# Kernel optimization log

Hardware: AMD Instinct MI355X
Metric: run time of the kernel (lower is better)

Reference implementation:

```python
import math
import jax, jax.numpy as jnp
import numpy as np

B, S, H, D = 2, 2048, 16, 64

def setup_inputs() -> dict:
    key = jax.random.key(0)
    qkv = jax.random.normal(key, (B, S, 3, H, D), dtype=jnp.float32)
    return {"qkv": qkv}

def reference(qkv) -> jnp.ndarray:
    # qkv: [B, S, 3, H, D]
    q = qkv[:, :, 0]  # [B, S, H, D]
    k = qkv[:, :, 1]
    v = qkv[:, :, 2]
    seqlen = qkv.shape[1]
    softmax_scale = 1.0 / math.sqrt(q.shape[-1])
    # scores: [B, H, T, S]
    scores = jnp.einsum('bthd,bshd->bhts', q, k * softmax_scale)
    # additive causal mask with -10000 above the diagonal (matches torch.triu(..., 1))
    causal_mask = jnp.triu(jnp.full((seqlen, seqlen), -10000.0, dtype=scores.dtype), 1)
    scores = scores + causal_mask
    attention = jax.nn.softmax(scores, axis=-1)
    # dropout_p = 0.0 (eval), so no dropout applied
    output = jnp.einsum('bhts,bshd->bthd', attention, v)  # [B, T, H, D]
    return output
```

## Files before the change

### kernel.cpp

```cpp
#include <hip/hip_runtime.h>

typedef __bf16 bf16x8 __attribute__((ext_vector_type(8)));
typedef float f32x4 __attribute__((ext_vector_type(4)));
typedef unsigned int u32;

constexpr int Bc = 2, Sc = 2048, Hc = 16, Dc = 64;
constexpr int QBLK = 64, KVBLK = 64;
constexpr int NT = Sc / QBLK;
constexpr int ROWSTR = 3 * Hc * Dc;
constexpr float QSCALE = 0.125f * 1.4426950408889634f;


template <int CTRL>
static __device__ __forceinline__ float dppf(float x) {
  int xi = __builtin_bit_cast(int, x);
  return __builtin_bit_cast(float,
      __builtin_amdgcn_update_dpp(xi, xi, CTRL, 0xF, 0xF, false));
}
static __device__ __forceinline__ float redmax16(float x) {
  x = fmaxf(x, dppf<0x121>(x));
  x = fmaxf(x, dppf<0x122>(x));
  x = fmaxf(x, dppf<0x124>(x));
  x = fmaxf(x, dppf<0x128>(x));
  return x;
}
static __device__ __forceinline__ float redsum16(float x) {
  x += dppf<0x121>(x);
  x += dppf<0x122>(x);
  x += dppf<0x124>(x);
  x += dppf<0x128>(x);
  return x;
}

static __device__ __forceinline__ u32 pack2(float a, float b) {
  unsigned short x = __builtin_bit_cast(unsigned short, (__bf16)a);
  unsigned short y = __builtin_bit_cast(unsigned short, (__bf16)b);
  return (u32)x | ((u32)y << 16);
}

__global__ __launch_bounds__(512, 4)
void fattn_kernel(const float* __restrict__ qkv, float* __restrict__ out) {
  const int id = blockIdx.x + blockIdx.y * gridDim.x;
  const int swz = (id & 7) * 64 + (id >> 3);
  const int xlow = swz & 15;
  const int xhigh = NT - 1 - xlow;
  const int bh = swz >> 4;
  const int b = bh >> 4, h = bh & 15;

  const int tid = threadIdx.x;
  const int wave = tid >> 6;
  const int lane = tid & 63;
  const int lg = lane >> 4;
  const int li = lane & 15;
  const bool is_h = wave < 4;
  const int sub = wave & 3;
  const int myx = is_h ? xhigh : xlow;
  const int qw = myx * QBLK + sub * 16;

  const float* qp = qkv + (size_t)b * Sc * ROWSTR + h * Dc;
  const float* kp = qp + Hc * Dc;
  const float* vp = qp + 2 * Hc * Dc;

  __shared__ __align__(16) char k_s[KVBLK * Dc * 2];
  __shared__ __align__(16) char v_s[Dc * KVBLK * 2];
  __shared__ __align__(16) char p_s[8][16 * KVBLK * 2];
  char* pw = p_s[wave];

  bf16x8 qf[2];
  {
    const float* qr = qp + (size_t)(qw + li) * ROWSTR + 8 * lg;
#pragma unroll
    for (int fi = 0; fi < 2; ++fi) {
      f32x4 a0 = *(const f32x4*)(qr + 32 * fi);
      f32x4 a1 = *(const f32x4*)(qr + 32 * fi + 4);
      bf16x8 qa;
#pragma unroll
      for (int j = 0; j < 4; ++j) {
        qa[j] = (__bf16)(a0[j] * QSCALE); qa[j + 4] = (__bf16)(a1[j] * QSCALE);
      }
      qf[fi] = qa;
    }
  }

  f32x4 oacc[4];
  float mrow[4], lrow[4];
#pragma unroll
  for (int n = 0; n < 4; ++n) oacc[n] = f32x4{0, 0, 0, 0};
#pragma unroll
  for (int r = 0; r < 4; ++r) { mrow[r] = -1e30f; lrow[r] = 0.f; }

  for (int t = 0; t <= xhigh; ++t) {
    const int kv0 = t * KVBLK;

    {
      const int r = tid >> 3, g = tid & 7;
      const float* ks = kp + (size_t)(kv0 + r) * ROWSTR + g * 8;
      const float* vs = vp + (size_t)(kv0 + r) * ROWSTR + g * 8;
      f32x4 k0 = *(const f32x4*)ks;
      f32x4 k1 = *(const f32x4*)(ks + 4);
      f32x4 v0 = *(const f32x4*)vs;
      f32x4 v1 = *(const f32x4*)(vs + 4);
      bf16x8 kb;
#pragma unroll
      for (int j = 0; j < 4; ++j) { kb[j] = (__bf16)k0[j]; kb[j + 4] = (__bf16)k1[j]; }
      *(bf16x8*)(k_s + ((r * 128 + g * 16) ^ ((r & 7) << 4))) = kb;

      const int odd = r & 1;
      f32x4 tmp = odd ? v0 : v1;
      f32x4 rcv;
#pragma unroll
      for (int j = 0; j < 4; ++j) rcv[j] = dppf<0x128>(tmp[j]);
      const int kvb2 = (r & ~1) * 2;
#pragma unroll
      for (int s = 0; s < 4; ++s) {
        const int dj = (s + g) & 3;
        const float lo = odd ? rcv[dj] : v0[dj];
        const float hi = odd ? v1[dj] : rcv[dj];
        const int d = 8 * g + 4 * odd + dj;
        *(u32*)(v_s + ((d * 128 + kvb2) ^ ((d & 7) << 4))) = pack2(lo, hi);
      }
    }
    __syncthreads();

    if (t <= myx) {
      f32x4 sacc[4];
#pragma unroll
      for (int n = 0; n < 4; ++n) sacc[n] = f32x4{0, 0, 0, 0};
      __builtin_amdgcn_s_setprio(1);
#pragma unroll
      for (int n = 0; n < 4; ++n) {
        const int krow = 16 * n + li;
        const int sw = (krow & 7) << 4;
#pragma unroll
        for (int fi = 0; fi < 2; ++fi) {
          bf16x8 kb = *(const bf16x8*)(k_s + ((krow * 128 + fi * 64 + lg * 16) ^ sw));
          sacc[n] = __builtin_amdgcn_mfma_f32_16x16x32_bf16(qf[fi], kb, sacc[n], 0, 0, 0);
        }
      }
      __builtin_amdgcn_s_setprio(0);

      if (t == myx) {
        const int qrow = qw + 4 * lg;
#pragma unroll
        for (int n = 0; n < 4; ++n)
#pragma unroll
          for (int r = 0; r < 4; ++r)
            if (kv0 + 16 * n + li > qrow + r) sacc[n][r] = -1e30f;
      }

      float pm[4];
#pragma unroll
      for (int r = 0; r < 4; ++r) {
        pm[r] = fmaxf(fmaxf(sacc[0][r], sacc[1][r]), fmaxf(sacc[2][r], sacc[3][r]));
        pm[r] = redmax16(pm[r]);
      }

      bool need = false;
#pragma unroll
      for (int r = 0; r < 4; ++r) need = need || (pm[r] > mrow[r] + 8.0f);
      if (__any(need)) {
#pragma unroll
        for (int r = 0; r < 4; ++r) {
          float mnew = fmaxf(mrow[r], pm[r]);
          float scl = __builtin_exp2f(mrow[r] - mnew);
          mrow[r] = mnew;
          lrow[r] *= scl;
#pragma unroll
          for (int n = 0; n < 4; ++n) oacc[n][r] *= scl;
        }
      }

#pragma unroll
      for (int r = 0; r < 4; ++r) {
        float s = 0.f;
#pragma unroll
        for (int n = 0; n < 4; ++n) {
          float p = __builtin_exp2f(sacc[n][r] - mrow[r]);
          sacc[n][r] = p;
          s += p;
        }
        lrow[r] += redsum16(s);
      }

      {
        const int oddli = li & 1;
        const int kvoff = (li & ~1) * 2;
        const int q0 = 4 * lg + 2 * oddli;
        const int sw0 = (q0 & 7) << 4;
        const int sw1 = ((q0 + 1) & 7) << 4;
#pragma unroll
        for (int n = 0; n < 4; ++n) {
          float t0 = oddli ? sacc[n][0] : sacc[n][2];
          float t1 = oddli ? sacc[n][1] : sacc[n][3];
          float r0 = dppf<0xB1>(t0);
          float r1 = dppf<0xB1>(t1);
          float lo0 = oddli ? r0 : sacc[n][0];
          float hi0 = oddli ? sacc[n][2] : r0;
          float lo1 = oddli ? r1 : sacc[n][1];
          float hi1 = oddli ? sacc[n][3] : r1;
          const int base = n * 32 + kvoff;
          *(u32*)(pw + ((q0 * 128 + base) ^ sw0)) = pack2(lo0, hi0);
          *(u32*)(pw + (((q0 + 1) * 128 + base) ^ sw1)) = pack2(lo1, hi1);
        }
      }

#pragma unroll
      for (int ks = 0; ks < 2; ++ks) {
        const int pbyte = (li * 128 + (32 * ks + 8 * lg) * 2) ^ ((li & 7) << 4);
        bf16x8 pa = *(const bf16x8*)(pw + pbyte);
        __builtin_amdgcn_s_setprio(1);
#pragma unroll
        for (int n = 0; n < 4; ++n) {
          const int row = 16 * n + li;
          const int vbyte = (row * 128 + (32 * ks + 8 * lg) * 2) ^ ((row & 7) << 4);
          bf16x8 vb = *(const bf16x8*)(v_s + vbyte);
          oacc[n] = __builtin_amdgcn_mfma_f32_16x16x32_bf16(pa, vb, oacc[n], 0, 0, 0);
        }
        __builtin_amdgcn_s_setprio(0);
      }
    }
    __syncthreads();
  }

#pragma unroll
  for (int r = 0; r < 4; ++r) {
    const float inv = 1.0f / lrow[r];
    float* op = out + ((size_t)(b * Sc + qw + 4 * lg + r) * Hc + h) * Dc;
#pragma unroll
    for (int n = 0; n < 4; ++n)
      op[16 * n + li] = oacc[n][r] * inv;
  }
}

extern "C" void kernel_launch(void* const* d_in, const int* in_sizes, int n_in,
                              void* d_out, int out_size, void* d_ws, size_t ws_size,
                              hipStream_t stream) {
  const float* qkv = (const float*)d_in[0];
  float* out = (float*)d_out;
  dim3 grid(NT / 2, Bc * Hc);
  fattn_kernel<<<grid, 512, 0, stream>>>(qkv, out);
}
```

Baseline: 94.74 us.

## Switch to 32x32x16 MFMA with transposed scores kept in registers

```diff
diff --git a/kernel.cpp b/kernel.cpp
--- a/kernel.cpp
+++ b/kernel.cpp
@@ -2,7 +2,9 @@
 
 typedef __bf16 bf16x8 __attribute__((ext_vector_type(8)));
 typedef float f32x4 __attribute__((ext_vector_type(4)));
+typedef float f32x16 __attribute__((ext_vector_type(16)));
 typedef unsigned int u32;
+typedef u32 u32x4 __attribute__((ext_vector_type(4)));
 
 constexpr int Bc = 2, Sc = 2048, Hc = 16, Dc = 64;
 constexpr int QBLK = 64, KVBLK = 64;
@@ -17,20 +19,6 @@
   return __builtin_bit_cast(float,
       __builtin_amdgcn_update_dpp(xi, xi, CTRL, 0xF, 0xF, false));
 }
-static __device__ __forceinline__ float redmax16(float x) {
-  x = fmaxf(x, dppf<0x121>(x));
-  x = fmaxf(x, dppf<0x122>(x));
-  x = fmaxf(x, dppf<0x124>(x));
-  x = fmaxf(x, dppf<0x128>(x));
-  return x;
-}
-static __device__ __forceinline__ float redsum16(float x) {
-  x += dppf<0x121>(x);
-  x += dppf<0x122>(x);
-  x += dppf<0x124>(x);
-  x += dppf<0x128>(x);
-  return x;
-}
 
 static __device__ __forceinline__ u32 pack2(float a, float b) {
   unsigned short x = __builtin_bit_cast(unsigned short, (__bf16)a);
@@ -38,7 +26,7 @@
   return (u32)x | ((u32)y << 16);
 }
 
-__global__ __launch_bounds__(512, 4)
+__global__ __launch_bounds__(256, 2)
 void fattn_kernel(const float* __restrict__ qkv, float* __restrict__ out) {
   const int id = blockIdx.x + blockIdx.y * gridDim.x;
   const int swz = (id & 7) * 64 + (id >> 3);
@@ -50,12 +38,12 @@
   const int tid = threadIdx.x;
   const int wave = tid >> 6;
   const int lane = tid & 63;
-  const int lg = lane >> 4;
-  const int li = lane & 15;
-  const bool is_h = wave < 4;
-  const int sub = wave & 3;
-  const int myx = is_h ? xhigh : xlow;
-  const int qw = myx * QBLK + sub * 16;
+  const int hh = lane >> 5;
+  const int q = lane & 31;
+
+  const int myx = (wave < 2) ? xhigh : xlow;
+  const int qw = myx * QBLK + (wave & 1) * 32;
+  const int myq = qw + q;
 
   const float* qp = qkv + (size_t)b * Sc * ROWSTR + h * Dc;
   const float* kp = qp + Hc * Dc;
@@ -63,37 +51,34 @@
 
   __shared__ __align__(16) char k_s[KVBLK * Dc * 2];
   __shared__ __align__(16) char v_s[Dc * KVBLK * 2];
-  __shared__ __align__(16) char p_s[8][16 * KVBLK * 2];
-  char* pw = p_s[wave];
-
-  bf16x8 qf[2];
-  {
-    const float* qr = qp + (size_t)(qw + li) * ROWSTR + 8 * lg;
-#pragma unroll
-    for (int fi = 0; fi < 2; ++fi) {
-      f32x4 a0 = *(const f32x4*)(qr + 32 * fi);
-      f32x4 a1 = *(const f32x4*)(qr + 32 * fi + 4);
-      bf16x8 qa;
-#pragma unroll
-      for (int j = 0; j < 4; ++j) {
-        qa[j] = (__bf16)(a0[j] * QSCALE); qa[j + 4] = (__bf16)(a1[j] * QSCALE);
-      }
-      qf[fi] = qa;
-    }
+
+  bf16x8 qf[4];
+#pragma unroll
+  for (int c = 0; c < 4; ++c) {
+    const float* qr = qp + (size_t)myq * ROWSTR + 16 * c + 8 * hh;
+    f32x4 a0 = *(const f32x4*)qr;
+    f32x4 a1 = *(const f32x4*)(qr + 4);
+    bf16x8 qa;
+#pragma unroll
+    for (int j = 0; j < 4; ++j) {
+      qa[j] = (__bf16)(a0[j] * QSCALE); qa[j + 4] = (__bf16)(a1[j] * QSCALE);
+    }
+    qf[c] = qa;
   }
 
-  f32x4 oacc[4];
-  float mrow[4], lrow[4];
-#pragma unroll
-  for (int n = 0; n < 4; ++n) oacc[n] = f32x4{0, 0, 0, 0};
-#pragma unroll
-  for (int r = 0; r < 4; ++r) { mrow[r] = -1e30f; lrow[r] = 0.f; }
+  f32x16 o0, o1;
+#pragma unroll
+  for (int i = 0; i < 16; ++i) { o0[i] = 0.f; o1[i] = 0.f; }
+  float mreg = -1e30f, lsum = 0.f;
+
+  const int swq = (q & 7) << 4;
 
   for (int t = 0; t <= xhigh; ++t) {
     const int kv0 = t * KVBLK;
 
-    {
-      const int r = tid >> 3, g = tid & 7;
+#pragma unroll
+    for (int it = 0; it < 2; ++it) {
+      const int u = tid + it * 256, r = u >> 3, g = u & 7;
       const float* ks = kp + (size_t)(kv0 + r) * ROWSTR + g * 8;
       const float* vs = vp + (size_t)(kv0 + r) * ROWSTR + g * 8;
       f32x4 k0 = *(const f32x4*)ks;
@@ -123,112 +108,112 @@
     __syncthreads();
 
     if (t <= myx) {
-      f32x4 sacc[4];
-#pragma unroll
-      for (int n = 0; n < 4; ++n) sacc[n] = f32x4{0, 0, 0, 0};
+      f32x16 p0, p1;
+#pragma unroll
+      for (int i = 0; i < 16; ++i) { p0[i] = 0.f; p1[i] = 0.f; }
       __builtin_amdgcn_s_setprio(1);
 #pragma unroll
-      for (int n = 0; n < 4; ++n) {
-        const int krow = 16 * n + li;
-        const int sw = (krow & 7) << 4;
-#pragma unroll
-        for (int fi = 0; fi < 2; ++fi) {
-          bf16x8 kb = *(const bf16x8*)(k_s + ((krow * 128 + fi * 64 + lg * 16) ^ sw));
-          sacc[n] = __builtin_amdgcn_mfma_f32_16x16x32_bf16(qf[fi], kb, sacc[n], 0, 0, 0);
+      for (int c = 0; c < 4; ++c) {
+        const int off = (16 * c + 8 * hh) * 2;
+        bf16x8 kf0 = *(const bf16x8*)(k_s + ((q * 128 + off) ^ swq));
+        bf16x8 kf1 = *(const bf16x8*)(k_s + (((32 + q) * 128 + off) ^ swq));
+        p0 = __builtin_amdgcn_mfma_f32_32x32x16_bf16(kf0, qf[c], p0, 0, 0, 0);
+        p1 = __builtin_amdgcn_mfma_f32_32x32x16_bf16(kf1, qf[c], p1, 0, 0, 0);
+      }
+      __builtin_amdgcn_s_setprio(0);
+
+      if (t == myx) {
+#pragma unroll
+        for (int r = 0; r < 16; ++r) {
+          const int kvl = (r & 3) + 8 * (r >> 2) + 4 * hh;
+          if (kv0 + kvl > myq) p0[r] = -1e30f;
+          if (kv0 + 32 + kvl > myq) p1[r] = -1e30f;
         }
       }
+
+      float tr[16];
+#pragma unroll
+      for (int i = 0; i < 16; ++i) tr[i] = fmaxf(p0[i], p1[i]);
+#pragma unroll
+      for (int s = 8; s > 0; s >>= 1)
+#pragma unroll
+        for (int i = 0; i < 8; ++i)
+          if (i < s) tr[i] = fmaxf(tr[i], tr[i + s]);
+      float pm = fmaxf(tr[0], __shfl_xor(tr[0], 32, 64));
+
+      if (__any(pm > mreg + 8.0f)) {
+        float mn = fmaxf(mreg, pm);
+        float scl = __builtin_exp2f(mreg - mn);
+        mreg = mn;
+        lsum *= scl;
+        o0 *= scl;
+        o1 *= scl;
+      }
+
+      float s0 = 0.f, s1 = 0.f, s2 = 0.f, s3 = 0.f;
+#pragma unroll
+      for (int i = 0; i < 16; ++i) {
+        p0[i] = __builtin_exp2f(p0[i] - mreg);
+        p1[i] = __builtin_exp2f(p1[i] - mreg);
+      }
+#pragma unroll
+      for (int i = 0; i < 4; ++i) {
+        s0 += p0[4 * i + 0] + p1[4 * i + 0];
+        s1 += p0[4 * i + 1] + p1[4 * i + 1];
+        s2 += p0[4 * i + 2] + p1[4 * i + 2];
+        s3 += p0[4 * i + 3] + p1[4 * i + 3];
+      }
+      lsum += (s0 + s1) + (s2 + s3);
+
+      bf16x8 pb[4];
+#pragma unroll
+      for (int c = 0; c < 4; ++c) {
+        const int m0 = 2 * (c & 1);
+        const f32x16& P = (c < 2) ? p0 : p1;
+        u32 A0 = pack2(P[4 * m0 + 0], P[4 * m0 + 1]);
+        u32 A1 = pack2(P[4 * m0 + 2], P[4 * m0 + 3]);
+        u32 B0 = pack2(P[4 * m0 + 4], P[4 * m0 + 5]);
+        u32 B1 = pack2(P[4 * m0 + 6], P[4 * m0 + 7]);
+        u32 snd0 = hh ? A0 : B0;
+        u32 snd1 = hh ? A1 : B1;
+        u32 rcv0 = (u32)__shfl_xor((int)snd0, 32, 64);
+        u32 rcv1 = (u32)__shfl_xor((int)snd1, 32, 64);
+        u32x4 f;
+        f[0] = hh ? rcv0 : A0;
+        f[1] = hh ? rcv1 : A1;
+        f[2] = hh ? B0 : rcv0;
+        f[3] = hh ? B1 : rcv1;
+        pb[c] = __builtin_bit_cast(bf16x8, f);
+      }
+
+      __builtin_amdgcn_s_setprio(1);
+#pragma unroll
+      for (int c = 0; c < 4; ++c) {
+        const int off = (16 * c + 8 * hh) * 2;
+        bf16x8 vf0 = *(const bf16x8*)(v_s + ((q * 128 + off) ^ swq));
+        bf16x8 vf1 = *(const bf16x8*)(v_s + (((32 + q) * 128 + off) ^ swq));
+        o0 = __builtin_amdgcn_mfma_f32_32x32x16_bf16(vf0, pb[c], o0, 0, 0, 0);
+        o1 = __builtin_amdgcn_mfma_f32_32x32x16_bf16(vf1, pb[c], o1, 0, 0, 0);
+      }
       __builtin_amdgcn_s_setprio(0);
-
-      if (t == myx) {
-        const int qrow = qw + 4 * lg;
-#pragma unroll
-        for (int n = 0; n < 4; ++n)
-#pragma unroll
-          for (int r = 0; r < 4; ++r)
-            if (kv0 + 16 * n + li > qrow + r) sacc[n][r] = -1e30f;
-      }
-
-      float pm[4];
-#pragma unroll
-      for (int r = 0; r < 4; ++r) {
-        pm[r] = fmaxf(fmaxf(sacc[0][r], sacc[1][r]), fmaxf(sacc[2][r], sacc[3][r]));
-        pm[r] = redmax16(pm[r]);
-      }
-
-      bool need = false;
-#pragma unroll
-      for (int r = 0; r < 4; ++r) need = need || (pm[r] > mrow[r] + 8.0f);
-      if (__any(need)) {
-#pragma unroll
-        for (int r = 0; r < 4; ++r) {
-          float mnew = fmaxf(mrow[r], pm[r]);
-          float scl = __builtin_exp2f(mrow[r] - mnew);
-          mrow[r] = mnew;
-          lrow[r] *= scl;
-#pragma unroll
-          for (int n = 0; n < 4; ++n) oacc[n][r] *= scl;
-        }
-      }
-
-#pragma unroll
-      for (int r = 0; r < 4; ++r) {
-        float s = 0.f;
-#pragma unroll
-        for (int n = 0; n < 4; ++n) {
-          float p = __builtin_exp2f(sacc[n][r] - mrow[r]);
-          sacc[n][r] = p;
-          s += p;
-        }
-        lrow[r] += redsum16(s);
-      }
-
-      {
-        const int oddli = li & 1;
-        const int kvoff = (li & ~1) * 2;
-        const int q0 = 4 * lg + 2 * oddli;
-        const int sw0 = (q0 & 7) << 4;
-        const int sw1 = ((q0 + 1) & 7) << 4;
-#pragma unroll
-        for (int n = 0; n < 4; ++n) {
-          float t0 = oddli ? sacc[n][0] : sacc[n][2];
-          float t1 = oddli ? sacc[n][1] : sacc[n][3];
-          float r0 = dppf<0xB1>(t0);
-          float r1 = dppf<0xB1>(t1);
-          float lo0 = oddli ? r0 : sacc[n][0];
-          float hi0 = oddli ? sacc[n][2] : r0;
-          float lo1 = oddli ? r1 : sacc[n][1];
-          float hi1 = oddli ? sacc[n][3] : r1;
-          const int base = n * 32 + kvoff;
-          *(u32*)(pw + ((q0 * 128 + base) ^ sw0)) = pack2(lo0, hi0);
-          *(u32*)(pw + (((q0 + 1) * 128 + base) ^ sw1)) = pack2(lo1, hi1);
-        }
-      }
-
-#pragma unroll
-      for (int ks = 0; ks < 2; ++ks) {
-        const int pbyte = (li * 128 + (32 * ks + 8 * lg) * 2) ^ ((li & 7) << 4);
-        bf16x8 pa = *(const bf16x8*)(pw + pbyte);
-        __builtin_amdgcn_s_setprio(1);
-#pragma unroll
-        for (int n = 0; n < 4; ++n) {
-          const int row = 16 * n + li;
-          const int vbyte = (row * 128 + (32 * ks + 8 * lg) * 2) ^ ((row & 7) << 4);
-          bf16x8 vb = *(const bf16x8*)(v_s + vbyte);
-          oacc[n] = __builtin_amdgcn_mfma_f32_16x16x32_bf16(pa, vb, oacc[n], 0, 0, 0);
-        }
-        __builtin_amdgcn_s_setprio(0);
-      }
     }
     __syncthreads();
   }
 
-#pragma unroll
-  for (int r = 0; r < 4; ++r) {
-    const float inv = 1.0f / lrow[r];
-    float* op = out + ((size_t)(b * Sc + qw + 4 * lg + r) * Hc + h) * Dc;
-#pragma unroll
-    for (int n = 0; n < 4; ++n)
-      op[16 * n + li] = oacc[n][r] * inv;
+  lsum += __shfl_xor(lsum, 32, 64);
+  const float inv = 1.0f / lsum;
+  float* op = out + ((size_t)(b * Sc + myq) * Hc + h) * Dc;
+#pragma unroll
+  for (int m = 0; m < 4; ++m) {
+    f32x4 w0, w1;
+#pragma unroll
+    for (int j = 0; j < 4; ++j) {
+      w0[j] = o0[4 * m + j] * inv;
+      w1[j] = o1[4 * m + j] * inv;
+    }
+    const int d0 = 8 * m + 4 * hh;
+    *(f32x4*)(op + d0) = w0;
+    *(f32x4*)(op + 32 + d0) = w1;
   }
 }
 
@@ -238,5 +223,5 @@
   const float* qkv = (const float*)d_in[0];
   float* out = (float*)d_out;
   dim3 grid(NT / 2, Bc * Hc);
-  fattn_kernel<<<grid, 512, 0, stream>>>(qkv, out);
-}
+  fattn_kernel<<<grid, 256, 0, stream>>>(qkv, out);
+}
```

Result: slower. 98.65 us (+4.1%).
